# Performance work log

Hardware: AMD Instinct MI355X
Metric: run time of the kernel (lower is better)

The kernel has to match this reference:

```python
import jax, jax.numpy as jnp
import numpy as np

N_NODES = 110
C = 4096  # in_channels = hidden = out_channels


def setup_inputs() -> dict:
    key = jax.random.key(0)
    ks = jax.random.split(key, 8)
    x = jax.random.normal(ks[0], (N_NODES, C), dtype=jnp.float32)
    adj = jax.random.randint(ks[1], (N_NODES, N_NODES), 0, 2, dtype=jnp.int32)
    # torch.nn.Linear weights stored [out_features, in_features]
    W2 = jax.random.normal(ks[2], (C, C), dtype=jnp.float32) / np.sqrt(C)
    b2 = jax.random.normal(ks[3], (C,), dtype=jnp.float32) * 0.01
    W1 = jax.random.normal(ks[4], (2 * C, C), dtype=jnp.float32) / np.sqrt(2 * C)
    b1 = jax.random.normal(ks[5], (C,), dtype=jnp.float32) * 0.01
    Wl = jax.random.normal(ks[6], (N_NODES, N_NODES), dtype=jnp.float32) / np.sqrt(N_NODES)
    bl = jax.random.normal(ks[7], (N_NODES,), dtype=jnp.float32) * 0.01
    # note: W1 is stored [in=2C, out=C]; W2 [in=C, out=C]; Wl [in=110, out=110]
    return {"x": x, "adj": adj, "W2": W2, "b2": b2, "W1": W1, "b1": b1, "Wl": Wl, "bl": bl}


def reference(x, adj, W2, b2, W1, b1, Wl, bl):
    # FeatGraphConv: h = lin2(x)
    h = x @ W2 + b2  # [N, C]
    # edge_index.nonzero(): adjacency -> edge list (i=src, j=dst); mean-aggregate
    # h[src] at dst. Dense equivalent: column-normalized mask matmul.
    mask = (adj != 0).astype(x.dtype)  # [N, N]
    deg = mask.sum(axis=0)  # in-degree of each target node j
    aggr = (mask.T @ h) / jnp.maximum(deg, 1.0)[:, None]  # [N, C]; 0 for isolated nodes (PyG mean)
    # update: lin1(cat(h, aggr)) then relu (in RegGNN.forward)
    out = jax.nn.relu(jnp.concatenate([h, aggr], axis=1) @ W1 + b1)  # [N, C]
    # x.t(); lin(110,110); x.t()
    out = (out.T @ Wl.T + bl).T  # [N, C]
    return out
```

## Files before the change

kernel.cpp:

```cpp
#include <hip/hip_runtime.h>
#include <hip/hip_fp16.h>

#define C 4096
#define NN 110
#define MPAD 112

typedef _Float16 f16x8 __attribute__((ext_vector_type(8)));
typedef float fx4 __attribute__((ext_vector_type(4)));
typedef unsigned long long ull;

__global__ __launch_bounds__(256)
void prep1_kernel(const float* __restrict__ x, _Float16* __restrict__ A1) {
    int idx = blockIdx.x * 256 + threadIdx.x;
    int n = idx >> 11;
    union { _Float16 h[2]; unsigned u; } pk;
    pk.u = 0;
    if (n < NN) {
        float2 v = *(const float2*)(x + 2 * (size_t)idx);
        pk.h[0] = (_Float16)v.x;
        pk.h[1] = (_Float16)v.y;
    }
    ((unsigned*)A1)[idx] = pk.u;
}

__global__ __launch_bounds__(128)
void maskprep_kernel(const int* __restrict__ adj, ull* __restrict__ mlo,
                     ull* __restrict__ mhi, float* __restrict__ degs) {
    int j = threadIdx.x;
    if (j < NN) {
        ull lo = 0, hi = 0; int dg = 0;
        for (int i = 0; i < 64; ++i) {
            int m = (adj[i * NN + j] != 0);
            lo |= ((ull)m) << i; dg += m;
        }
        for (int i = 64; i < NN; ++i) {
            int m = (adj[i * NN + j] != 0);
            hi |= ((ull)m) << (i - 64); dg += m;
        }
        mlo[j] = lo; mhi[j] = hi;
        degs[j] = (float)(dg > 0 ? dg : 1);
    }
}

#define PIPE_BARRIER()                                                \
    do {                                                              \
        asm volatile("s_waitcnt lgkmcnt(0)" ::: "memory");            \
        __builtin_amdgcn_s_barrier();                                 \
        __builtin_amdgcn_sched_barrier(0);                            \
    } while (0)

template<int NITER>
__global__ __launch_bounds__(256, 3)
void mm_kernel(const _Float16* __restrict__ A, const float* __restrict__ B,
               float* __restrict__ Cacc, int lda) {
    __shared__ __align__(16) _Float16 Bs[2][64 * 64];

    const int t   = threadIdx.x;
    const int j0  = blockIdx.x * 64;
    const int k0  = blockIdx.y * (NITER * 64);
    const int w   = t >> 6;
    const int L   = t & 63;
    const int l15 = L & 15;
    const int q   = L >> 4;
    const int sc  = t & 63;
    const int kg  = t >> 6;
    const int swz = sc & 7;

    fx4 acc[7];
#pragma unroll
    for (int mt = 0; mt < 7; ++mt) acc[mt] = (fx4){0.f, 0.f, 0.f, 0.f};

    const float*    Bp  = B + (size_t)k0 * C + j0 + sc;
    const _Float16* Ap  = A + (size_t)l15 * lda + k0;
    _Float16*       BsW = &Bs[0][0] + sc * 64;
    const _Float16* BsR = &Bs[0][0] + (w * 16 + l15) * 64;

    float bva[16], bvb[16];

#define LOADB(dst, ch)                                                         \
    { _Pragma("unroll")                                                        \
      for (int p = 0; p < 16; ++p)                                             \
          dst[p] = Bp[(size_t)((ch) * 64 + kg * 16 + p) * C]; }

#define COMMITB(src, buf)                                                      \
    { _Pragma("unroll")                                                        \
      for (int p2 = 0; p2 < 2; ++p2) {                                         \
          f16x8 hv;                                                            \
          _Pragma("unroll")                                                    \
          for (int e = 0; e < 8; ++e) hv[e] = (_Float16)src[p2 * 8 + e];       \
          *(f16x8*)(BsW + (buf) * 4096 + (((kg * 2 + p2) ^ swz) << 3)) = hv;   \
      } }

    LOADB(bva, 0);
    COMMITB(bva, 0);
    LOADB(bva, 1);
    PIPE_BARRIER();

#pragma unroll
    for (int it = 0; it < NITER; ++it) {
        f16x8 af[2][7];
#pragma unroll
        for (int s = 0; s < 2; ++s)
#pragma unroll
            for (int mt = 0; mt < 7; ++mt)
                af[s][mt] = *(const f16x8*)(Ap + (size_t)mt * 16 * lda
                                            + it * 64 + s * 32 + q * 8);
        __builtin_amdgcn_sched_barrier(0);
        if (it + 2 < NITER) {
            if (it & 1) { LOADB(bva, it + 2); } else { LOADB(bvb, it + 2); }
        }
        __builtin_amdgcn_sched_barrier(0);
#pragma unroll
        for (int s = 0; s < 2; ++s) {
            f16x8 bf = *(const f16x8*)(BsR + (it & 1) * 4096
                            + ((((s << 2) + q) ^ (l15 & 7)) << 3));
#pragma unroll
            for (int mt = 0; mt < 7; ++mt)
                acc[mt] = __builtin_amdgcn_mfma_f32_16x16x32_f16(
                    af[s][mt], bf, acc[mt], 0, 0, 0);
        }
        if (it + 1 < NITER) {
            if (it & 1) { COMMITB(bvb, (it + 1) & 1); }
            else        { COMMITB(bva, (it + 1) & 1); }
            PIPE_BARRIER();
        }
    }

    const int col = j0 + w * 16 + l15;
#pragma unroll
    for (int mt = 0; mt < 7; ++mt)
#pragma unroll
        for (int r = 0; r < 4; ++r) {
            int row = mt * 16 + q * 4 + r;
            if (row < NN)
                atomicAdd(&Cacc[(size_t)row * C + col], acc[mt][r]);
        }
#undef LOADB
#undef COMMITB
}

__global__ __launch_bounds__(256)
void agg_kernel(const float* __restrict__ h_raw, const ull* __restrict__ gmlo,
                const ull* __restrict__ gmhi, const float* __restrict__ gdegs,
                const float* __restrict__ b2, _Float16* __restrict__ A3) {
    __shared__ float hb[NN * 16];
    const int t  = threadIdx.x;
    const int c0 = blockIdx.x * 16;

    for (int idx = t; idx < NN * 8; idx += 256) {
        int n = idx >> 3, cp = (idx & 7) << 1;
        float2 v = *(const float2*)(h_raw + (size_t)n * C + c0 + cp);
        float v0 = v.x + b2[c0 + cp];
        float v1 = v.y + b2[c0 + cp + 1];
        hb[n * 16 + cp]     = v0;
        hb[n * 16 + cp + 1] = v1;
        union { _Float16 h[2]; unsigned u; } pk;
        pk.h[0] = (_Float16)v0;
        pk.h[1] = (_Float16)v1;
        *(unsigned*)(A3 + (size_t)n * (2 * C) + c0 + cp) = pk.u;
    }
    if (t < 32) {
        int n  = NN + (t >> 4);
        int hs = (t >> 3) & 1;
        int cp = (t & 7) << 1;
        *(unsigned*)(A3 + (size_t)n * (2 * C) + hs * C + c0 + cp) = 0u;
    }
    __syncthreads();
    for (int idx = t; idx < NN * 8; idx += 256) {
        int j = idx >> 3, cp = (idx & 7) << 1;
        ull lo = gmlo[j], hi = gmhi[j];
        float dg = gdegs[j];
        float a0 = 0.f, a1 = 0.f;
        for (int i = 0; i < 64; ++i)
            if ((lo >> i) & 1) { a0 += hb[i * 16 + cp]; a1 += hb[i * 16 + cp + 1]; }
        for (int i = 64; i < NN; ++i)
            if ((hi >> (i - 64)) & 1) { a0 += hb[i * 16 + cp]; a1 += hb[i * 16 + cp + 1]; }
        union { _Float16 h[2]; unsigned u; } pk;
        pk.h[0] = (_Float16)(a0 / dg);
        pk.h[1] = (_Float16)(a1 / dg);
        *(unsigned*)(A3 + (size_t)j * (2 * C) + C + c0 + cp) = pk.u;
    }
}

__global__ __launch_bounds__(256)
void fin_kernel(const float* __restrict__ z_raw, const float* __restrict__ b1,
                const float* __restrict__ Wl, const float* __restrict__ bl,
                float* __restrict__ out) {
    __shared__ float zs[NN * 64];
    const int t  = threadIdx.x;
    const int c0 = blockIdx.x * 64;
    const int c  = t & 63;

    for (int idx = t; idx < NN * 64; idx += 256) {
        int k = idx >> 6, cc = idx & 63;
        float v = z_raw[(size_t)k * C + c0 + cc] + b1[c0 + cc];
        zs[idx] = fmaxf(v, 0.f);
    }
    __syncthreads();
    for (int jj = 0; jj < 7; ++jj) {
        int j = blockIdx.y * 28 + jj * 4 + (t >> 6);
        if (j < NN) {
            float a = bl[j];
#pragma unroll 2
            for (int k = 0; k < NN; ++k)
                a += Wl[j * NN + k] * zs[k * 64 + c];
            out[(size_t)j * C + c0 + c] = a;
        }
    }
}

extern "C" void kernel_launch(void* const* d_in, const int* in_sizes, int n_in,
                              void* d_out, int out_size, void* d_ws, size_t ws_size,
                              hipStream_t stream) {
    const float* x   = (const float*)d_in[0];
    const int*   adj = (const int*)d_in[1];
    const float* W2  = (const float*)d_in[2];
    const float* b2  = (const float*)d_in[3];
    const float* W1  = (const float*)d_in[4];
    const float* b1  = (const float*)d_in[5];
    const float* Wl  = (const float*)d_in[6];
    const float* bl  = (const float*)d_in[7];
    float* out = (float*)d_out;

    char* ws = (char*)d_ws;
    float*    h_raw = (float*)(ws);
    float*    z_raw = (float*)(ws + 1802240);
    _Float16* A1    = (_Float16*)(ws + 3604480);
    _Float16* A3    = (_Float16*)(ws + 4521984);
    ull*      mlo   = (ull*)(ws + 6356992);
    ull*      mhi   = (ull*)(ws + 6357872);
    float*    degs  = (float*)(ws + 6358752);

    hipMemsetAsync(d_ws, 0, 3604480, stream);
    prep1_kernel<<<(MPAD * C / 2) / 256, 256, 0, stream>>>(x, A1);
    maskprep_kernel<<<1, 128, 0, stream>>>(adj, mlo, mhi, degs);
    mm_kernel<4><<<dim3(64, 16), 256, 0, stream>>>(A1, W2, h_raw, C);
    agg_kernel<<<C / 16, 256, 0, stream>>>(h_raw, mlo, mhi, degs, b2, A3);
    mm_kernel<8><<<dim3(64, 16), 256, 0, stream>>>(A3, W1, z_raw, 2 * C);
    fin_kernel<<<dim3(C / 64, 4), 256, 0, stream>>>(z_raw, b1, Wl, bl, out);
}
```

Before: 392.3 us.

## Pre-swizzle A operand into MFMA fragment layout and stage it through LDS

The producer kernels now write the fp16 activation matrices in an MFMA-fragment-tiled layout. The GEMM kernel loads A tiles cooperatively with contiguous 16-byte loads into double-buffered shared memory, replacing per-wave strided global fragment loads. B loading also changes to float2 reads covering two columns per thread. The aim is fewer, coalesced global loads and A reuse across the four waves, at the cost of more LDS traffic and capacity, which may reduce occupancy.

```diff
diff --git a/kernel.cpp b/kernel.cpp
--- a/kernel.cpp
+++ b/kernel.cpp
@@ -4,23 +4,33 @@
 #define C 4096
 #define NN 110
 #define MPAD 112
+#define NMT 7
+#define KBS (NMT * 512)
 
 typedef _Float16 f16x8 __attribute__((ext_vector_type(8)));
 typedef float fx4 __attribute__((ext_vector_type(4)));
 typedef unsigned long long ull;
 
+
 __global__ __launch_bounds__(256)
-void prep1_kernel(const float* __restrict__ x, _Float16* __restrict__ A1) {
-    int idx = blockIdx.x * 256 + threadIdx.x;
-    int n = idx >> 11;
-    union { _Float16 h[2]; unsigned u; } pk;
-    pk.u = 0;
+void prep1_kernel(const float* __restrict__ x, _Float16* __restrict__ A1t) {
+    int u = blockIdx.x * 256 + threadIdx.x;
+    int kb  = u / 448;
+    int rem = u - kb * 448;
+    int mt  = rem >> 6;
+    int L   = rem & 63;
+    int n   = mt * 16 + (L & 15);
+    int c   = kb * 32 + (L >> 4) * 8;
+    f16x8 hv;
     if (n < NN) {
-        float2 v = *(const float2*)(x + 2 * (size_t)idx);
-        pk.h[0] = (_Float16)v.x;
-        pk.h[1] = (_Float16)v.y;
-    }
-    ((unsigned*)A1)[idx] = pk.u;
+        float4 v0 = *(const float4*)(x + (size_t)n * C + c);
+        float4 v1 = *(const float4*)(x + (size_t)n * C + c + 4);
+        hv[0]=(_Float16)v0.x; hv[1]=(_Float16)v0.y; hv[2]=(_Float16)v0.z; hv[3]=(_Float16)v0.w;
+        hv[4]=(_Float16)v1.x; hv[5]=(_Float16)v1.y; hv[6]=(_Float16)v1.z; hv[7]=(_Float16)v1.w;
+    } else {
+        for (int e = 0; e < 8; ++e) hv[e] = (_Float16)0.f;
+    }
+    *(f16x8*)(A1t + (size_t)u * 8) = hv;
 }
 
 __global__ __launch_bounds__(128)
@@ -52,59 +62,68 @@
 template<int NITER>
 __global__ __launch_bounds__(256, 3)
 void mm_kernel(const _Float16* __restrict__ A, const float* __restrict__ B,
-               float* __restrict__ Cacc, int lda) {
+               float* __restrict__ Cacc) {
+    __shared__ __align__(16) _Float16 As[2][2 * KBS];
     __shared__ __align__(16) _Float16 Bs[2][64 * 64];
 
     const int t   = threadIdx.x;
     const int j0  = blockIdx.x * 64;
-    const int k0  = blockIdx.y * (NITER * 64);
+    const int kb0 = blockIdx.y * (NITER * 2);
     const int w   = t >> 6;
     const int L   = t & 63;
     const int l15 = L & 15;
     const int q   = L >> 4;
-    const int sc  = t & 63;
-    const int kg  = t >> 6;
-    const int swz = sc & 7;
+    const int sc2 = (t & 31) * 2;
+    const int kgr = (t >> 5) & 7;
 
     fx4 acc[7];
 #pragma unroll
     for (int mt = 0; mt < 7; ++mt) acc[mt] = (fx4){0.f, 0.f, 0.f, 0.f};
 
-    const float*    Bp  = B + (size_t)k0 * C + j0 + sc;
-    const _Float16* Ap  = A + (size_t)l15 * lda + k0;
-    _Float16*       BsW = &Bs[0][0] + sc * 64;
+    const float*    Bp  = B + (size_t)blockIdx.y * (NITER * 64) * C + j0 + sc2;
+    const _Float16* ApC = A + (size_t)kb0 * KBS;
     const _Float16* BsR = &Bs[0][0] + (w * 16 + l15) * 64;
-
-    float bva[16], bvb[16];
+    const _Float16* AsR = &As[0][0];
+
+    f16x8  av[4];
+    float2 bva[8], bvb[8];
+
+#define LOADA(ch)                                                              \
+    { _Pragma("unroll")                                                        \
+      for (int i = 0; i < 4; ++i)                                              \
+          if (i < 3 || t < 128)                                                \
+              av[i] = *(const f16x8*)(ApC + (size_t)(ch) * (2 * KBS)           \
+                                      + (t + i * 256) * 8); }
+
+#define COMMITA(buf)                                                           \
+    { _Pragma("unroll")                                                        \
+      for (int i = 0; i < 4; ++i)                                              \
+          if (i < 3 || t < 128)                                                \
+              *(f16x8*)(&As[buf][0] + (t + i * 256) * 8) = av[i]; }
 
 #define LOADB(dst, ch)                                                         \
     { _Pragma("unroll")                                                        \
-      for (int p = 0; p < 16; ++p)                                             \
-          dst[p] = Bp[(size_t)((ch) * 64 + kg * 16 + p) * C]; }
+      for (int p = 0; p < 8; ++p)                                              \
+          dst[p] = *(const float2*)(Bp + (size_t)((ch) * 64 + kgr * 8 + p) * C); }
 
 #define COMMITB(src, buf)                                                      \
-    { _Pragma("unroll")                                                        \
-      for (int p2 = 0; p2 < 2; ++p2) {                                         \
-          f16x8 hv;                                                            \
-          _Pragma("unroll")                                                    \
-          for (int e = 0; e < 8; ++e) hv[e] = (_Float16)src[p2 * 8 + e];       \
-          *(f16x8*)(BsW + (buf) * 4096 + (((kg * 2 + p2) ^ swz) << 3)) = hv;   \
-      } }
-
+    { f16x8 h0, h1;                                                            \
+      _Pragma("unroll")                                                        \
+      for (int e = 0; e < 8; ++e) { h0[e] = (_Float16)src[e].x;                \
+                                    h1[e] = (_Float16)src[e].y; }              \
+      *(f16x8*)(&Bs[buf][0] + sc2 * 64 + ((kgr ^ (sc2 & 7)) << 3)) = h0;       \
+      *(f16x8*)(&Bs[buf][0] + (sc2 + 1) * 64 + ((kgr ^ ((sc2 + 1) & 7)) << 3)) = h1; }
+
+    LOADA(0);
     LOADB(bva, 0);
+    COMMITA(0);
     COMMITB(bva, 0);
     LOADB(bva, 1);
     PIPE_BARRIER();
 
 #pragma unroll
     for (int it = 0; it < NITER; ++it) {
-        f16x8 af[2][7];
-#pragma unroll
-        for (int s = 0; s < 2; ++s)
-#pragma unroll
-            for (int mt = 0; mt < 7; ++mt)
-                af[s][mt] = *(const f16x8*)(Ap + (size_t)mt * 16 * lda
-                                            + it * 64 + s * 32 + q * 8);
+        if (it + 1 < NITER) LOADA(it + 1);
         __builtin_amdgcn_sched_barrier(0);
         if (it + 2 < NITER) {
             if (it & 1) { LOADB(bva, it + 2); } else { LOADB(bvb, it + 2); }
@@ -115,11 +134,15 @@
             f16x8 bf = *(const f16x8*)(BsR + (it & 1) * 4096
                             + ((((s << 2) + q) ^ (l15 & 7)) << 3));
 #pragma unroll
-            for (int mt = 0; mt < 7; ++mt)
+            for (int mt = 0; mt < 7; ++mt) {
+                f16x8 afrag = *(const f16x8*)(AsR + (it & 1) * (2 * KBS)
+                                  + (s * 7 + mt) * 512 + L * 8);
                 acc[mt] = __builtin_amdgcn_mfma_f32_16x16x32_f16(
-                    af[s][mt], bf, acc[mt], 0, 0, 0);
+                    afrag, bf, acc[mt], 0, 0, 0);
+            }
         }
         if (it + 1 < NITER) {
+            COMMITA((it + 1) & 1);
             if (it & 1) { COMMITB(bvb, (it + 1) & 1); }
             else        { COMMITB(bva, (it + 1) & 1); }
             PIPE_BARRIER();
@@ -135,14 +158,21 @@
             if (row < NN)
                 atomicAdd(&Cacc[(size_t)row * C + col], acc[mt][r]);
         }
+#undef LOADA
+#undef COMMITA
 #undef LOADB
 #undef COMMITB
+}
+
+__device__ __forceinline__ size_t fragidx(int n, int c) {
+    return (size_t)(c >> 5) * KBS + (n >> 4) * 512
+         + (((c >> 3) & 3) * 16 + (n & 15)) * 8 + (c & 7);
 }
 
 __global__ __launch_bounds__(256)
 void agg_kernel(const float* __restrict__ h_raw, const ull* __restrict__ gmlo,
                 const ull* __restrict__ gmhi, const float* __restrict__ gdegs,
-                const float* __restrict__ b2, _Float16* __restrict__ A3) {
+                const float* __restrict__ b2, _Float16* __restrict__ A3t) {
     __shared__ float hb[NN * 16];
     const int t  = threadIdx.x;
     const int c0 = blockIdx.x * 16;
@@ -157,13 +187,13 @@
         union { _Float16 h[2]; unsigned u; } pk;
         pk.h[0] = (_Float16)v0;
         pk.h[1] = (_Float16)v1;
-        *(unsigned*)(A3 + (size_t)n * (2 * C) + c0 + cp) = pk.u;
+        *(unsigned*)(A3t + fragidx(n, c0 + cp)) = pk.u;
     }
     if (t < 32) {
-        int n  = NN + (t >> 4);
-        int hs = (t >> 3) & 1;
+        int n  = 110 + ((t >> 3) & 1);
+        int hs = t >> 4;
         int cp = (t & 7) << 1;
-        *(unsigned*)(A3 + (size_t)n * (2 * C) + hs * C + c0 + cp) = 0u;
+        *(unsigned*)(A3t + fragidx(n, hs * C + c0 + cp)) = 0u;
     }
     __syncthreads();
     for (int idx = t; idx < NN * 8; idx += 256) {
@@ -178,7 +208,7 @@
         union { _Float16 h[2]; unsigned u; } pk;
         pk.h[0] = (_Float16)(a0 / dg);
         pk.h[1] = (_Float16)(a1 / dg);
-        *(unsigned*)(A3 + (size_t)j * (2 * C) + C + c0 + cp) = pk.u;
+        *(unsigned*)(A3t + fragidx(j, C + c0 + cp)) = pk.u;
     }
 }
 
@@ -225,17 +255,17 @@
     char* ws = (char*)d_ws;
     float*    h_raw = (float*)(ws);
     float*    z_raw = (float*)(ws + 1802240);
-    _Float16* A1    = (_Float16*)(ws + 3604480);
-    _Float16* A3    = (_Float16*)(ws + 4521984);
+    _Float16* A1t   = (_Float16*)(ws + 3604480);
+    _Float16* A3t   = (_Float16*)(ws + 4521984);
     ull*      mlo   = (ull*)(ws + 6356992);
     ull*      mhi   = (ull*)(ws + 6357872);
     float*    degs  = (float*)(ws + 6358752);
 
     hipMemsetAsync(d_ws, 0, 3604480, stream);
-    prep1_kernel<<<(MPAD * C / 2) / 256, 256, 0, stream>>>(x, A1);
+    prep1_kernel<<<224, 256, 0, stream>>>(x, A1t);
     maskprep_kernel<<<1, 128, 0, stream>>>(adj, mlo, mhi, degs);
-    mm_kernel<4><<<dim3(64, 16), 256, 0, stream>>>(A1, W2, h_raw, C);
-    agg_kernel<<<C / 16, 256, 0, stream>>>(h_raw, mlo, mhi, degs, b2, A3);
-    mm_kernel<8><<<dim3(64, 16), 256, 0, stream>>>(A3, W1, z_raw, 2 * C);
+    mm_kernel<4><<<dim3(64, 16), 256, 0, stream>>>(A1t, W2, h_raw);
+    agg_kernel<<<C / 16, 256, 0, stream>>>(h_raw, mlo, mhi, degs, b2, A3t);
+    mm_kernel<8><<<dim3(64, 16), 256, 0, stream>>>(A3t, W1, z_raw);
     fin_kernel<<<dim3(C / 64, 4), 256, 0, stream>>>(z_raw, b1, Wl, bl, out);
 }
```

Result: faster. 355.5 us (-9.4%).
